# Performance work log

Measured on AMD Instinct MI355X. Metric: run time of the kernel, lower is better.

Reference implementation:

```python
import jax, jax.numpy as jnp
import numpy as np

NUM_HEADS = 16
HEAD_DIM = 64
CONTEXT = 128


def setup_inputs() -> dict:
    key = jax.random.key(0)
    k1, k2, k3, k4, k5 = jax.random.split(key, 5)
    B, S, H = 4, 4096, 1024
    inputs = jax.random.normal(k1, (B, S, H), dtype=jnp.float32)
    attention_mask = jnp.ones((B, S), dtype=jnp.int32)
    s = 1.0 / np.sqrt(H)
    Wq = jax.random.normal(k2, (H, H), dtype=jnp.float32) * s
    Wk = jax.random.normal(k3, (H, H), dtype=jnp.float32) * s
    Wv = jax.random.normal(k4, (H, H), dtype=jnp.float32) * s
    Wo = jax.random.normal(k5, (H, H), dtype=jnp.float32) * s
    return {"inputs": inputs, "attention_mask": attention_mask,
            "Wq": Wq, "Wk": Wk, "Wv": Wv, "Wo": Wo}


def reference(inputs, attention_mask, Wq, Wk, Wv, Wo):
    B, S, H = inputs.shape
    nH, dh = NUM_HEADS, HEAD_DIM
    C = min(CONTEXT, S)
    ctx_start = max(0, S - C)
    scale = 1.0 / np.sqrt(dh)

    # Q from all positions; K/V only from the recent context window
    q = (inputs @ Wq.T).reshape(B, S, nH, dh).transpose(0, 2, 1, 3)      # [B,nH,S,dh]
    ctx_in = inputs[:, ctx_start:, :]                                    # [B,C,H]
    k = (ctx_in @ Wk.T).reshape(B, C, nH, dh).transpose(0, 2, 1, 3)      # [B,nH,C,dh]
    v = (ctx_in @ Wv.T).reshape(B, C, nH, dh).transpose(0, 2, 1, 3)      # [B,nH,C,dh]

    scores = jnp.einsum('bhsd,bhcd->bhsc', q, k) * scale                 # [B,nH,S,C]

    # causal mask: context position <= query position; queries strictly
    # before the context window may attend to the first context token
    qpos = jnp.arange(S)
    cpos = jnp.arange(ctx_start, ctx_start + C)
    causal = cpos[None, :] <= qpos[:, None]                              # [S,C]
    before = qpos < ctx_start
    causal = causal.at[:, 0].set(causal[:, 0] | before)
    mask = causal[None, None, :, :]                                      # [1,1,S,C]

    # padding mask on context tokens
    ctx_pad = (attention_mask[:, ctx_start:ctx_start + C] != 0)          # [B,C]
    mask = mask & ctx_pad[:, None, None, :]

    scores = jnp.where(mask, scores, -jnp.inf)
    weights = jax.nn.softmax(scores, axis=-1)

    out = jnp.einsum('bhsc,bhcd->bhsd', weights, v)                      # [B,nH,S,dh]
    out = out.transpose(0, 2, 1, 3).reshape(B, S, H)
    return out @ Wo.T
```

## Files before the change

kernel.cpp:

```cpp
#include <hip/hip_runtime.h>
#include <math.h>

#define B_ 4
#define S_ 4096
#define H_ 1024
#define NH 16
#define DH 64
#define CTX 128
#define CSTART (S_ - CTX)
#define KDIM 1024

typedef __attribute__((ext_vector_type(8))) short short8;
typedef __attribute__((ext_vector_type(4))) float floatx4;
typedef unsigned short ushort_t;

__device__ inline unsigned short f2bf(float x) {
    union { float f; unsigned u; } v; v.f = x;
    unsigned r = v.u + 0x7fffu + ((v.u >> 16) & 1u);
    return (unsigned short)(r >> 16);
}

__device__ inline uint4 pack8(float4 a, float4 b) {
    union { unsigned short us[8]; uint4 u4; } p;
    p.us[0]=f2bf(a.x); p.us[1]=f2bf(a.y); p.us[2]=f2bf(a.z); p.us[3]=f2bf(a.w);
    p.us[4]=f2bf(b.x); p.us[5]=f2bf(b.y); p.us[6]=f2bf(b.z); p.us[7]=f2bf(b.w);
    return p.u4;
}

#define GLOAD_LDS16(g, l) \
    __builtin_amdgcn_global_load_lds((__attribute__((address_space(1))) const void*)(g), \
                                     (__attribute__((address_space(3))) void*)(l), 16, 0, 0)

__global__ __launch_bounds__(256) void prep(const float* __restrict__ in,
                                            const float* __restrict__ Wq, const float* __restrict__ Wk,
                                            const float* __restrict__ Wv, const float* __restrict__ Wo,
                                            ushort_t* __restrict__ Wbf, ushort_t* __restrict__ Xs) {
    int bx = blockIdx.x;
    if (bx < 2048) {
        size_t idx = (size_t)bx * 256 + threadIdx.x;
        size_t e = idx * 8;
        int wsel = (int)(e >> 20);
        size_t off = e & 1048575;
        const float* src = wsel == 0 ? Wq : wsel == 1 ? Wk : wsel == 2 ? Wv : Wo;
        const float4* s4 = (const float4*)(src + off);
        *(uint4*)(Wbf + e) = pack8(s4[0], s4[1]);
    } else {
        int idx = (bx - 2048) * 256 + threadIdx.x;
        int e = idx * 8;
        int m = e >> 10;
        int col = e & 1023;
        int b = m >> 7, i = m & 127;
        const float4* s4 = (const float4*)(in + (size_t)(b * S_ + CSTART + i) * H_ + col);
        *(uint4*)(Xs + e) = pack8(s4[0], s4[1]);
    }
}

template<int MODE>
__global__ __launch_bounds__(256) void gemm_t(const ushort_t* __restrict__ A,
                                              const ushort_t* __restrict__ W,
                                              void* __restrict__ Cv,
                                              float* __restrict__ rbuf, int ldc) {
    __shared__ ushort_t As[2][4096];
    __shared__ ushort_t Bs[2][4096];
    int tid = threadIdx.x;
    int lane = tid & 63, w = tid >> 6;
    int m0 = blockIdx.y * 64, n0 = blockIdx.x * 64;
    int f0 = tid, f1 = tid + 256;
    int r0 = f0 >> 3, g0 = (f0 & 7) ^ (r0 & 7);
    int r1 = f1 >> 3, g1 = (f1 & 7) ^ (r1 & 7);
    const ushort_t* ga0 = A + (size_t)(m0 + r0) * KDIM + g0 * 8;
    const ushort_t* ga1 = A + (size_t)(m0 + r1) * KDIM + g1 * 8;
    const ushort_t* gb0 = W + (size_t)(n0 + r0) * KDIM + g0 * 8;
    const ushort_t* gb1 = W + (size_t)(n0 + r1) * KDIM + g1 * 8;
    char* la0[2] = { (char*)&As[0][0] + f0 * 16, (char*)&As[1][0] + f0 * 16 };
    char* la1[2] = { (char*)&As[0][0] + f1 * 16, (char*)&As[1][0] + f1 * 16 };
    char* lb0[2] = { (char*)&Bs[0][0] + f0 * 16, (char*)&Bs[1][0] + f0 * 16 };
    char* lb1[2] = { (char*)&Bs[0][0] + f1 * 16, (char*)&Bs[1][0] + f1 * 16 };
    int fm = lane & 15, q = lane >> 4;
    int wr = w >> 1, wc = w & 1;
    int ma0 = wr * 32, na0 = wc * 32;
    floatx4 acc[2][2] = {};
    GLOAD_LDS16(ga0, la0[0]);
    GLOAD_LDS16(ga1, la1[0]);
    GLOAD_LDS16(gb0, lb0[0]);
    GLOAD_LDS16(gb1, lb1[0]);
    for (int it = 0; it < KDIM / 64; it++) {
        __syncthreads();
        int buf = it & 1;
        if (it + 1 < KDIM / 64) {
            int ko = (it + 1) * 64;
            GLOAD_LDS16(ga0 + ko, la0[buf ^ 1]);
            GLOAD_LDS16(ga1 + ko, la1[buf ^ 1]);
            GLOAD_LDS16(gb0 + ko, lb0[buf ^ 1]);
            GLOAD_LDS16(gb1 + ko, lb1[buf ^ 1]);
        }
        const ushort_t* as = &As[buf][0];
        const ushort_t* bs = &Bs[buf][0];
        #pragma unroll
        for (int kb = 0; kb < 2; kb++) {
            short8 af[2], bfr[2];
            #pragma unroll
            for (int t = 0; t < 2; t++) {
                int m = ma0 + t * 16 + fm;
                int pa = (kb * 4 + q) ^ (m & 7);
                af[t] = *(const short8*)&as[m * 64 + pa * 8];
                int n = na0 + t * 16 + fm;
                int pb = (kb * 4 + q) ^ (n & 7);
                bfr[t] = *(const short8*)&bs[n * 64 + pb * 8];
            }
            #pragma unroll
            for (int i = 0; i < 2; i++)
                #pragma unroll
                for (int j = 0; j < 2; j++)
                    acc[i][j] = __builtin_amdgcn_mfma_f32_16x16x32_bf16(af[i], bfr[j], acc[i][j], 0, 0, 0);
        }
    }
    #pragma unroll
    for (int i = 0; i < 2; i++)
        #pragma unroll
        for (int j = 0; j < 2; j++) {
            int rowg = m0 + ma0 + i * 16 + q * 4;
            int col = n0 + na0 + j * 16 + fm;
            #pragma unroll
            for (int t = 0; t < 4; t++) {
                float val = acc[i][j][t];
                if (MODE == 0) {
                    ((float*)Cv)[(size_t)(rowg + t) * ldc + col] = val;
                } else if (MODE == 1) {
                    ((ushort_t*)Cv)[(size_t)(rowg + t) * ldc + col] = f2bf(val);
                } else {
                    int m = rowg + t;
                    int b = m >> 7, p = m & 127;
                    ((float*)Cv)[(size_t)(b * S_ + CSTART + p) * H_ + col] = val;
                    if (p == 0) rbuf[b * H_ + col] = val;
                }
            }
        }
}

__global__ __launch_bounds__(512) void attn(const ushort_t* __restrict__ QKV,
                                            const int* __restrict__ amask,
                                            ushort_t* __restrict__ AO) {
    __shared__ __align__(16) char smem[55296];
    ushort_t* Qs  = (ushort_t*)(smem);
    ushort_t* Ksh = (ushort_t*)(smem + 18432);
    ushort_t* Pb  = (ushort_t*)(smem);
    float*    linv = (float*)(smem + 36864);
    int*      amk  = (int*)(smem + 37376);
    ushort_t* Vt   = (ushort_t*)(smem + 37888);

    int b = blockIdx.x >> 4;
    int h = blockIdx.x & 15;
    int tid = threadIdx.x;
    {
        int r = tid >> 2, ch = tid & 3;
        const ushort_t* base = QKV + (size_t)(b * CTX + r) * 3072 + h * 64 + ch * 16;
        uint4 q0 = *(const uint4*)(base);
        uint4 q1 = *(const uint4*)(base + 8);
        *(uint4*)(Qs + r * 72 + ch * 16)     = q0;
        *(uint4*)(Qs + r * 72 + ch * 16 + 8) = q1;
        uint4 k0 = *(const uint4*)(base + 1024);
        uint4 k1 = *(const uint4*)(base + 1024 + 8);
        *(uint4*)(Ksh + r * 72 + ch * 16)     = k0;
        *(uint4*)(Ksh + r * 72 + ch * 16 + 8) = k1;
        union { uint4 u4[2]; ushort_t us[16]; } vv;
        vv.u4[0] = *(const uint4*)(base + 2048);
        vv.u4[1] = *(const uint4*)(base + 2048 + 8);
        #pragma unroll
        for (int i = 0; i < 16; i++)
            Vt[(ch * 16 + i) * 136 + r] = vv.us[i];
        if (tid < 128) amk[tid] = amask[b * S_ + CSTART + tid];
    }
    __syncthreads();

    int w = tid >> 6, lane = tid & 63;
    int qt = w;
    int fm = lane & 15, quad = lane >> 4;

    short8 af[2];
    #pragma unroll
    for (int kb = 0; kb < 2; kb++)
        af[kb] = *(const short8*)(Qs + (qt * 16 + fm) * 72 + kb * 32 + quad * 8);
    floatx4 acc[8] = {};
    for (int ct = 0; ct <= qt; ct++) {
        #pragma unroll
        for (int kb = 0; kb < 2; kb++) {
            short8 bfr = *(const short8*)(Ksh + (ct * 16 + fm) * 72 + kb * 32 + quad * 8);
            acc[ct] = __builtin_amdgcn_mfma_f32_16x16x32_bf16(af[kb], bfr, acc[ct], 0, 0, 0);
        }
    }
    int myamk[8];
    #pragma unroll
    for (int ct = 0; ct < 8; ct++) myamk[ct] = amk[ct * 16 + fm];
    float ls[4];
    #pragma unroll
    for (int t = 0; t < 4; t++) {
        int row = qt * 16 + quad * 4 + t;
        float m = -INFINITY;
        #pragma unroll
        for (int ct = 0; ct < 8; ct++) {
            int col = ct * 16 + fm;
            float s = acc[ct][t] * 0.125f;
            bool valid = (ct <= qt) && (col <= row) && (myamk[ct] != 0);
            if (valid) m = fmaxf(m, s);
        }
        #pragma unroll
        for (int off = 8; off >= 1; off >>= 1) m = fmaxf(m, __shfl_xor(m, off, 64));
        float l = 0.f;
        #pragma unroll
        for (int ct = 0; ct < 8; ct++) {
            int col = ct * 16 + fm;
            float s = acc[ct][t] * 0.125f;
            bool valid = (ct <= qt) && (col <= row) && (myamk[ct] != 0);
            float p = valid ? __expf(s - m) : 0.f;
            acc[ct][t] = p;
            l += p;
        }
        #pragma unroll
        for (int off = 8; off >= 1; off >>= 1) l += __shfl_xor(l, off, 64);
        ls[t] = l;
    }
    __syncthreads();
    #pragma unroll
    for (int t = 0; t < 4; t++) {
        int row = qt * 16 + quad * 4 + t;
        #pragma unroll
        for (int ct = 0; ct < 8; ct++)
            Pb[row * 136 + ct * 16 + fm] = f2bf(acc[ct][t]);
        if (fm == 0) linv[row] = 1.f / ls[t];
    }
    int kmax = (qt >> 1) + 1;
    floatx4 oacc[4] = {};
    for (int kb = 0; kb < kmax; kb++) {
        short8 paf = *(const short8*)(Pb + (qt * 16 + fm) * 136 + kb * 32 + quad * 8);
        #pragma unroll
        for (int dt = 0; dt < 4; dt++) {
            short8 vbf = *(const short8*)(Vt + (dt * 16 + fm) * 136 + kb * 32 + quad * 8);
            oacc[dt] = __builtin_amdgcn_mfma_f32_16x16x32_bf16(paf, vbf, oacc[dt], 0, 0, 0);
        }
    }
    #pragma unroll
    for (int t = 0; t < 4; t++) {
        int row = qt * 16 + quad * 4 + t;
        float inv = linv[row];
        #pragma unroll
        for (int dt = 0; dt < 4; dt++)
            AO[(size_t)(b * CTX + row) * H_ + h * 64 + dt * 16 + fm] = f2bf(oacc[dt][t] * inv);
    }
}

__global__ __launch_bounds__(256) void write_bcast(const float* __restrict__ rbuf,
                                                   float* __restrict__ out) {
    size_t idx = (size_t)blockIdx.x * 256 + threadIdx.x;
    int b   = (int)(idx / (CSTART * 256));
    int rem = (int)(idx % (CSTART * 256));
    int p   = rem >> 8;
    int c4  = rem & 255;
    float4 v = ((const float4*)(rbuf + (size_t)b * H_))[c4];
    ((float4*)(out + (size_t)(b * S_ + p) * H_))[c4] = v;
}

extern "C" void kernel_launch(void* const* d_in, const int* in_sizes, int n_in,
                              void* d_out, int out_size, void* d_ws, size_t ws_size,
                              hipStream_t stream) {
    const float* inputs = (const float*)d_in[0];
    const int*   amask  = (const int*)d_in[1];
    const float* Wq     = (const float*)d_in[2];
    const float* Wk     = (const float*)d_in[3];
    const float* Wv     = (const float*)d_in[4];
    const float* Wo     = (const float*)d_in[5];
    float* out = (float*)d_out;

    char* ws = (char*)d_ws;
    ushort_t* Xs   = (ushort_t*)(ws);
    ushort_t* Wbf  = (ushort_t*)(ws + (1u << 20));
    ushort_t* QKV  = (ushort_t*)(ws + (9u << 20));
    ushort_t* AObf = (ushort_t*)(ws + (13u << 20));
    float*    rbuf = (float*)(ws + (14u << 20));

    prep<<<2304, 256, 0, stream>>>(inputs, Wq, Wk, Wv, Wo, Wbf, Xs);

    dim3 gq(3072 / 64, 512 / 64);
    gemm_t<1><<<gq, 256, 0, stream>>>(Xs, Wbf, (void*)QKV, nullptr, 3072);

    attn<<<64, 512, 0, stream>>>(QKV, amask, AObf);

    dim3 go(1024 / 64, 512 / 64);
    gemm_t<2><<<go, 256, 0, stream>>>(AObf, Wbf + (size_t)3072 * 1024, (void*)out, rbuf, H_);

    write_bcast<<<(B_ * CSTART * 256) / 256, 256, 0, stream>>>(rbuf, out);
}
```

Baseline: 159.4 us.

## Split-K both projection GEMMs and reduce partials in consumer kernels

Both GEMMs are split along K into two halves via a third grid dimension, doubling the block count for better CU occupancy on small M. Each half writes fp32 partials. The attention kernel sums the two halves and converts to bf16, and a new assemble kernel sums the output partials and writes every output row, replacing the separate broadcast kernel. The GEMM loop also drops LDS double buffering in favour of single-buffer load-sync-compute-sync. This adds fp32 partial traffic and removes the overlap of loads with compute.

Result: faster. 153.3 us (-3.9%).

```diff
diff --git a/kernel.cpp b/kernel.cpp
--- a/kernel.cpp
+++ b/kernel.cpp
@@ -9,6 +9,7 @@
 #define CTX 128
 #define CSTART (S_ - CTX)
 #define KDIM 1024
+#define KH 512
 
 typedef __attribute__((ext_vector_type(8))) short short8;
 typedef __attribute__((ext_vector_type(4))) float floatx4;
@@ -25,6 +26,10 @@
     p.us[0]=f2bf(a.x); p.us[1]=f2bf(a.y); p.us[2]=f2bf(a.z); p.us[3]=f2bf(a.w);
     p.us[4]=f2bf(b.x); p.us[5]=f2bf(b.y); p.us[6]=f2bf(b.z); p.us[7]=f2bf(b.w);
     return p.u4;
+}
+
+__device__ inline float4 add4(float4 a, float4 b) {
+    float4 r; r.x=a.x+b.x; r.y=a.y+b.y; r.z=a.z+b.z; r.w=a.w+b.w; return r;
 }
 
 #define GLOAD_LDS16(g, l) \
@@ -55,47 +60,36 @@
     }
 }
 
-template<int MODE>
-__global__ __launch_bounds__(256) void gemm_t(const ushort_t* __restrict__ A,
-                                              const ushort_t* __restrict__ W,
-                                              void* __restrict__ Cv,
-                                              float* __restrict__ rbuf, int ldc) {
-    __shared__ ushort_t As[2][4096];
-    __shared__ ushort_t Bs[2][4096];
+__global__ __launch_bounds__(256) void gemm_part(const ushort_t* __restrict__ A,
+                                                 const ushort_t* __restrict__ W,
+                                                 float* __restrict__ P, int N) {
+    __shared__ ushort_t As[64][64];
+    __shared__ ushort_t Bs[64][64];
     int tid = threadIdx.x;
     int lane = tid & 63, w = tid >> 6;
     int m0 = blockIdx.y * 64, n0 = blockIdx.x * 64;
+    int ks = blockIdx.z;
     int f0 = tid, f1 = tid + 256;
     int r0 = f0 >> 3, g0 = (f0 & 7) ^ (r0 & 7);
     int r1 = f1 >> 3, g1 = (f1 & 7) ^ (r1 & 7);
-    const ushort_t* ga0 = A + (size_t)(m0 + r0) * KDIM + g0 * 8;
-    const ushort_t* ga1 = A + (size_t)(m0 + r1) * KDIM + g1 * 8;
-    const ushort_t* gb0 = W + (size_t)(n0 + r0) * KDIM + g0 * 8;
-    const ushort_t* gb1 = W + (size_t)(n0 + r1) * KDIM + g1 * 8;
-    char* la0[2] = { (char*)&As[0][0] + f0 * 16, (char*)&As[1][0] + f0 * 16 };
-    char* la1[2] = { (char*)&As[0][0] + f1 * 16, (char*)&As[1][0] + f1 * 16 };
-    char* lb0[2] = { (char*)&Bs[0][0] + f0 * 16, (char*)&Bs[1][0] + f0 * 16 };
-    char* lb1[2] = { (char*)&Bs[0][0] + f1 * 16, (char*)&Bs[1][0] + f1 * 16 };
+    const ushort_t* ga0 = A + (size_t)(m0 + r0) * KDIM + ks * KH + g0 * 8;
+    const ushort_t* ga1 = A + (size_t)(m0 + r1) * KDIM + ks * KH + g1 * 8;
+    const ushort_t* gb0 = W + (size_t)(n0 + r0) * KDIM + ks * KH + g0 * 8;
+    const ushort_t* gb1 = W + (size_t)(n0 + r1) * KDIM + ks * KH + g1 * 8;
+    char* la0 = (char*)As + f0 * 16;
+    char* la1 = (char*)As + f1 * 16;
+    char* lb0 = (char*)Bs + f0 * 16;
+    char* lb1 = (char*)Bs + f1 * 16;
     int fm = lane & 15, q = lane >> 4;
     int wr = w >> 1, wc = w & 1;
     int ma0 = wr * 32, na0 = wc * 32;
     floatx4 acc[2][2] = {};
-    GLOAD_LDS16(ga0, la0[0]);
-    GLOAD_LDS16(ga1, la1[0]);
-    GLOAD_LDS16(gb0, lb0[0]);
-    GLOAD_LDS16(gb1, lb1[0]);
-    for (int it = 0; it < KDIM / 64; it++) {
+    for (int k0 = 0; k0 < KH; k0 += 64) {
+        GLOAD_LDS16(ga0 + k0, la0);
+        GLOAD_LDS16(ga1 + k0, la1);
+        GLOAD_LDS16(gb0 + k0, lb0);
+        GLOAD_LDS16(gb1 + k0, lb1);
         __syncthreads();
-        int buf = it & 1;
-        if (it + 1 < KDIM / 64) {
-            int ko = (it + 1) * 64;
-            GLOAD_LDS16(ga0 + ko, la0[buf ^ 1]);
-            GLOAD_LDS16(ga1 + ko, la1[buf ^ 1]);
-            GLOAD_LDS16(gb0 + ko, lb0[buf ^ 1]);
-            GLOAD_LDS16(gb1 + ko, lb1[buf ^ 1]);
-        }
-        const ushort_t* as = &As[buf][0];
-        const ushort_t* bs = &Bs[buf][0];
         #pragma unroll
         for (int kb = 0; kb < 2; kb++) {
             short8 af[2], bfr[2];
@@ -103,10 +97,10 @@
             for (int t = 0; t < 2; t++) {
                 int m = ma0 + t * 16 + fm;
                 int pa = (kb * 4 + q) ^ (m & 7);
-                af[t] = *(const short8*)&as[m * 64 + pa * 8];
+                af[t] = *(const short8*)&As[m][pa * 8];
                 int n = na0 + t * 16 + fm;
                 int pb = (kb * 4 + q) ^ (n & 7);
-                bfr[t] = *(const short8*)&bs[n * 64 + pb * 8];
+                bfr[t] = *(const short8*)&Bs[n][pb * 8];
             }
             #pragma unroll
             for (int i = 0; i < 2; i++)
@@ -114,31 +108,22 @@
                 for (int j = 0; j < 2; j++)
                     acc[i][j] = __builtin_amdgcn_mfma_f32_16x16x32_bf16(af[i], bfr[j], acc[i][j], 0, 0, 0);
         }
-    }
+        __syncthreads();
+    }
+    float* outp = P + (size_t)ks * 512 * N;
     #pragma unroll
     for (int i = 0; i < 2; i++)
         #pragma unroll
         for (int j = 0; j < 2; j++) {
-            int rowg = m0 + ma0 + i * 16 + q * 4;
+            int row = m0 + ma0 + i * 16 + q * 4;
             int col = n0 + na0 + j * 16 + fm;
             #pragma unroll
-            for (int t = 0; t < 4; t++) {
-                float val = acc[i][j][t];
-                if (MODE == 0) {
-                    ((float*)Cv)[(size_t)(rowg + t) * ldc + col] = val;
-                } else if (MODE == 1) {
-                    ((ushort_t*)Cv)[(size_t)(rowg + t) * ldc + col] = f2bf(val);
-                } else {
-                    int m = rowg + t;
-                    int b = m >> 7, p = m & 127;
-                    ((float*)Cv)[(size_t)(b * S_ + CSTART + p) * H_ + col] = val;
-                    if (p == 0) rbuf[b * H_ + col] = val;
-                }
-            }
-        }
-}
-
-__global__ __launch_bounds__(512) void attn(const ushort_t* __restrict__ QKV,
+            for (int t = 0; t < 4; t++)
+                outp[(size_t)(row + t) * N + col] = acc[i][j][t];
+        }
+}
+
+__global__ __launch_bounds__(512) void attn(const float* __restrict__ Pq,
                                             const int* __restrict__ amask,
                                             ushort_t* __restrict__ AO) {
     __shared__ __align__(16) char smem[55296];
@@ -154,21 +139,26 @@
     int tid = threadIdx.x;
     {
         int r = tid >> 2, ch = tid & 3;
-        const ushort_t* base = QKV + (size_t)(b * CTX + r) * 3072 + h * 64 + ch * 16;
-        uint4 q0 = *(const uint4*)(base);
-        uint4 q1 = *(const uint4*)(base + 8);
-        *(uint4*)(Qs + r * 72 + ch * 16)     = q0;
-        *(uint4*)(Qs + r * 72 + ch * 16 + 8) = q1;
-        uint4 k0 = *(const uint4*)(base + 1024);
-        uint4 k1 = *(const uint4*)(base + 1024 + 8);
-        *(uint4*)(Ksh + r * 72 + ch * 16)     = k0;
-        *(uint4*)(Ksh + r * 72 + ch * 16 + 8) = k1;
-        union { uint4 u4[2]; ushort_t us[16]; } vv;
-        vv.u4[0] = *(const uint4*)(base + 2048);
-        vv.u4[1] = *(const uint4*)(base + 2048 + 8);
+        size_t base = (size_t)(b * CTX + r) * 3072 + h * 64 + ch * 16;
+        const float4* p0 = (const float4*)(Pq + base);
+        const float4* p1 = (const float4*)(Pq + (size_t)512 * 3072 + base);
+        float4 a0 = add4(p0[0], p1[0]), a1 = add4(p0[1], p1[1]);
+        float4 a2 = add4(p0[2], p1[2]), a3 = add4(p0[3], p1[3]);
+        *(uint4*)(Qs + r * 72 + ch * 16)     = pack8(a0, a1);
+        *(uint4*)(Qs + r * 72 + ch * 16 + 8) = pack8(a2, a3);
+        a0 = add4(p0[256], p1[256]); a1 = add4(p0[257], p1[257]);
+        a2 = add4(p0[258], p1[258]); a3 = add4(p0[259], p1[259]);
+        *(uint4*)(Ksh + r * 72 + ch * 16)     = pack8(a0, a1);
+        *(uint4*)(Ksh + r * 72 + ch * 16 + 8) = pack8(a2, a3);
+        float vv[16];
+        #pragma unroll
+        for (int c4 = 0; c4 < 4; c4++) {
+            float4 s = add4(p0[512 + c4], p1[512 + c4]);
+            vv[c4*4+0]=s.x; vv[c4*4+1]=s.y; vv[c4*4+2]=s.z; vv[c4*4+3]=s.w;
+        }
         #pragma unroll
         for (int i = 0; i < 16; i++)
-            Vt[(ch * 16 + i) * 136 + r] = vv.us[i];
+            Vt[(ch * 16 + i) * 136 + r] = f2bf(vv[i]);
         if (tid < 128) amk[tid] = amask[b * S_ + CSTART + tid];
     }
     __syncthreads();
@@ -249,15 +239,18 @@
     }
 }
 
-__global__ __launch_bounds__(256) void write_bcast(const float* __restrict__ rbuf,
-                                                   float* __restrict__ out) {
+__global__ __launch_bounds__(256) void assemble(const float* __restrict__ Po,
+                                                float* __restrict__ out) {
     size_t idx = (size_t)blockIdx.x * 256 + threadIdx.x;
-    int b   = (int)(idx / (CSTART * 256));
-    int rem = (int)(idx % (CSTART * 256));
-    int p   = rem >> 8;
-    int c4  = rem & 255;
-    float4 v = ((const float4*)(rbuf + (size_t)b * H_))[c4];
-    ((float4*)(out + (size_t)(b * S_ + p) * H_))[c4] = v;
+    int row = (int)(idx >> 8);
+    int c4  = (int)(idx & 255);
+    int b = row >> 12;
+    int p = row & 4095;
+    int lr = (p < CSTART) ? 0 : (p - CSTART);
+    size_t o = (size_t)(b * CTX + lr) * H_ + c4 * 4;
+    float4 v0 = *(const float4*)(Po + o);
+    float4 v1 = *(const float4*)(Po + (size_t)512 * H_ + o);
+    ((float4*)out)[idx] = add4(v0, v1);
 }
 
 extern "C" void kernel_launch(void* const* d_in, const int* in_sizes, int n_in,
@@ -274,19 +267,19 @@
     char* ws = (char*)d_ws;
     ushort_t* Xs   = (ushort_t*)(ws);
     ushort_t* Wbf  = (ushort_t*)(ws + (1u << 20));
-    ushort_t* QKV  = (ushort_t*)(ws + (9u << 20));
-    ushort_t* AObf = (ushort_t*)(ws + (13u << 20));
-    float*    rbuf = (float*)(ws + (14u << 20));
+    float*    Pq   = (float*)(ws + (9u << 20));
+    ushort_t* AObf = (ushort_t*)(ws + (23u << 20));
+    float*    Po   = (float*)(ws + (24u << 20));
 
     prep<<<2304, 256, 0, stream>>>(inputs, Wq, Wk, Wv, Wo, Wbf, Xs);
 
-    dim3 gq(3072 / 64, 512 / 64);
-    gemm_t<1><<<gq, 256, 0, stream>>>(Xs, Wbf, (void*)QKV, nullptr, 3072);
-
-    attn<<<64, 512, 0, stream>>>(QKV, amask, AObf);
-
-    dim3 go(1024 / 64, 512 / 64);
-    gemm_t<2><<<go, 256, 0, stream>>>(AObf, Wbf + (size_t)3072 * 1024, (void*)out, rbuf, H_);
-
-    write_bcast<<<(B_ * CSTART * 256) / 256, 256, 0, stream>>>(rbuf, out);
-}
+    dim3 gq(3072 / 64, 512 / 64, 2);
+    gemm_part<<<gq, 256, 0, stream>>>(Xs, Wbf, Pq, 3072);
+
+    attn<<<64, 512, 0, stream>>>(Pq, amask, AObf);
+
+    dim3 go(1024 / 64, 512 / 64, 2);
+    gemm_part<<<go, 256, 0, stream>>>(AObf, Wbf + (size_t)3072 * 1024, Po, 1024);
+
+    assemble<<<16384, 256, 0, stream>>>(Po, out);
+}
```
